# Kernel optimization log

Hardware: AMD Instinct MI355X
Metric: run time of the kernel (lower is better)

Reference implementation:

```python
import jax, jax.numpy as jnp
import numpy as np

NUM_NODES = 4
D = 1024            # hidden dim and dims of s_0, s_1; initial_input_dims = [D, D, 2D]
NUM_OPS = 5         # candidate ops per MixedLayer: linear, relu, tanh, sigmoid, leaky_relu(0.2)
NUM_LAYERS = 18     # sum_{i<4} (i+3)
BATCH = 4096

_ACTS = [
    lambda h: h,
    jax.nn.relu,
    jnp.tanh,
    jax.nn.sigmoid,
    lambda h: jax.nn.leaky_relu(h, 0.2),
]

def setup_inputs() -> dict:
    key = jax.random.key(0)
    ks = jax.random.split(key, 7)
    s_0 = jax.random.normal(ks[0], (BATCH, D), jnp.float32)
    s_1 = jax.random.normal(ks[1], (BATCH, D), jnp.float32)
    genotype = jax.random.uniform(ks[2], (NUM_LAYERS, NUM_OPS), jnp.float32)
    genotype = genotype / genotype.sum(-1, keepdims=True)  # softmax-like arch weights
    scale = 1.0 / np.sqrt(D)
    # 14 layers take a D-dim input; 4 layers (the cat(s_0,s_1) edge of each node) take 2D
    Ws = jax.random.normal(ks[3], (14, NUM_OPS, D, D), jnp.float32) * scale
    Wb = jax.random.normal(ks[4], (4, NUM_OPS, 2 * D, D), jnp.float32) * (scale / np.sqrt(2.0))
    bs = jax.random.normal(ks[5], (NUM_LAYERS, NUM_OPS, D), jnp.float32) * 0.01
    return {"s_0": s_0, "s_1": s_1, "genotype": genotype, "Ws": Ws, "Wb": Wb, "bs": bs}

def _mixed(x, W, b, w):
    # x: [B, in], W: [K, in, D], b: [K, D], w: [K]
    h = jnp.einsum('bi,kio->kbo', x, W) + b[:, None, :]
    out = 0.0
    for k, act in enumerate(_ACTS):
        out = out + w[k] * act(h[k])
    return out

def reference(s_0, s_1, genotype, Ws, Wb, bs):
    states = [s_0, s_1, jnp.concatenate([s_0, s_1], axis=-1)]
    offset, si, bi = 0, 0, 0
    for i in range(NUM_NODES):
        s = 0.0
        for j, cur in enumerate(states):
            l = offset + j
            if j == 2:  # edge from cat(s_0, s_1): input dim 2D
                W = Wb[bi]; bi += 1
            else:
                W = Ws[si]; si += 1
            s = s + _mixed(cur, W, bs[l], genotype[l])
        offset += len(states)
        states.append(s)
    return states[-1]
```

## Files before the change

### kernel.cpp

```cpp
#include <hip/hip_runtime.h>
#include <hip/hip_bf16.h>
#include <cstdint>
#include <cstddef>

typedef __attribute__((ext_vector_type(8))) short bf16x8;
typedef __attribute__((ext_vector_type(4))) float f32x4;

#define DEV __device__ __forceinline__

DEV unsigned short f2bf(float f) {
  unsigned int u = __float_as_uint(f);
  return (unsigned short)((u + 0x7fffu + ((u >> 16) & 1u)) >> 16);
}

DEV void gl_lds16(const unsigned short* g, unsigned short* l) {
  __builtin_amdgcn_global_load_lds(
      (__attribute__((address_space(1))) const void*)g,
      (__attribute__((address_space(3))) void*)l, 16, 0, 0);
}

__global__ __launch_bounds__(256) void cvt_kernel(const float* __restrict__ src,
                                                  unsigned short* __restrict__ dst) {
  size_t i = (size_t)blockIdx.x * 256 + threadIdx.x;
  float4 v = ((const float4*)src)[i];
  ushort4 o;
  o.x = f2bf(v.x); o.y = f2bf(v.y); o.z = f2bf(v.z); o.w = f2bf(v.w);
  ((ushort4*)dst)[i] = o;
}

__global__ __launch_bounds__(256) void zero_kernel(float* __restrict__ p) {
  size_t i = (size_t)blockIdx.x * 256 + threadIdx.x;
  ((float4*)p)[i] = make_float4(0.f, 0.f, 0.f, 0.f);
}

__global__ __launch_bounds__(256) void cvtzero_kernel(float* __restrict__ s,
                                                      unsigned short* __restrict__ dst) {
  size_t i = (size_t)blockIdx.x * 256 + threadIdx.x;
  float4 v = ((float4*)s)[i];
  ushort4 o;
  o.x = f2bf(v.x); o.y = f2bf(v.y); o.z = f2bf(v.z); o.w = f2bf(v.w);
  ((ushort4*)dst)[i] = o;
  ((float4*)s)[i] = make_float4(0.f, 0.f, 0.f, 0.f);
}

__global__ __launch_bounds__(256) void transpose_kernel(const float* __restrict__ src,
                                                        unsigned short* __restrict__ dst,
                                                        int K) {
  __shared__ float tile[64][68];
  const int t = threadIdx.x;
  const int tpm = (K >> 6) * 16;
  const int mat = blockIdx.x / tpm;
  const int r = blockIdx.x % tpm;
  const int tk = r >> 4;
  const int tn = r & 15;
  const size_t sbase = (size_t)mat * K * 1024 + (size_t)tk * 64 * 1024 + (size_t)tn * 64;
#pragma unroll
  for (int p = 0; p < 4; ++p) {
    int row = p * 16 + (t >> 4);
    int c4 = (t & 15) * 4;
    float4 v = *(const float4*)&src[sbase + (size_t)row * 1024 + c4];
    *(float4*)&tile[row][c4] = v;
  }
  __syncthreads();
  const int kbase = tk * 64;
  const size_t dbase = (size_t)mat * 1024 * K + (size_t)(kbase >> 10) * 1024 * 1024 +
                       (size_t)tn * 64 * 1024 + (size_t)(kbase & 1023);
#pragma unroll
  for (int p = 0; p < 4; ++p) {
    int n = p * 16 + (t >> 4);
    int k4 = (t & 15) * 4;
    ushort4 o;
    o.x = f2bf(tile[k4 + 0][n]);
    o.y = f2bf(tile[k4 + 1][n]);
    o.z = f2bf(tile[k4 + 2][n]);
    o.w = f2bf(tile[k4 + 3][n]);
    *(ushort4*)&dst[dbase + (size_t)n * 1024 + k4] = o;
  }
}

struct SegCfg {
  const unsigned short* x;
  const unsigned short* w;
  size_t wops;
  int l;
  int last;
};
struct NodeArgs {
  SegCfg s[7];
  int nseg;
};

#define PIPE_STEP(BUF, SA, SB)                                                   \
  {                                                                              \
    asm volatile("s_waitcnt vmcnt(12)" ::: "memory");                            \
    __builtin_amdgcn_s_barrier();                                                \
    __builtin_amdgcn_sched_barrier(0);                                           \
    bf16x8 af[4], bfr[4];                                                        \
    _Pragma("unroll") for (int mi = 0; mi < 4; ++mi)                             \
        af[mi] = *(const bf16x8*)&lds[(BUF) * 8192 + aof[mi]];                   \
    _Pragma("unroll") for (int ni = 0; ni < 4; ++ni)                             \
        bfr[ni] = *(const bf16x8*)&lds[(BUF) * 8192 + 4096 + bof[ni]];           \
    asm volatile("s_waitcnt lgkmcnt(0)" ::: "memory");                           \
    __builtin_amdgcn_sched_barrier(0);                                           \
    __builtin_amdgcn_s_barrier();                                                \
    __builtin_amdgcn_sched_barrier(0);                                           \
    {                                                                            \
      unsigned short* da = lds + (BUF) * 8192 + t * 8;                           \
      gl_lds16((SA), da);                                                        \
      gl_lds16((SA) + 64 * 1024, da + 2048);                                     \
      gl_lds16((SB), da + 4096);                                                 \
      gl_lds16((SB) + 64 * 1024, da + 6144);                                     \
    }                                                                            \
    _Pragma("unroll") for (int mi = 0; mi < 4; ++mi)                             \
        _Pragma("unroll") for (int ni = 0; ni < 4; ++ni)                         \
            hacc[mi][ni] = __builtin_amdgcn_mfma_f32_16x16x32_bf16(              \
                af[mi], bfr[ni], hacc[mi][ni], 0, 0, 0);                         \
  }

template <int NSEG>
__global__ __launch_bounds__(256, 2) void node_gemm(NodeArgs na,
                                                    const float* __restrict__ genotype,
                                                    const float* __restrict__ bs,
                                                    float* __restrict__ sout) {
  __shared__ unsigned short lds[32768];

  const int t = threadIdx.x;
  const int lane = t & 63;
  const int w = t >> 6;
  const int wm = (w & 1) * 64;
  const int wn = (w >> 1) * 64;
  const int bn = blockIdx.x * 128;
  const int bm = blockIdx.y * 128;
  const int kop = blockIdx.z;
  const int l15 = lane & 15;
  const int l16 = lane >> 4;

  const int srow = ((t >> 5) << 3) | (t & 7);
  const int schunk = (t >> 3) & 3;
  const size_t aoffg = (size_t)(bm + srow) * 1024 + schunk * 8;
  const size_t boffg = (size_t)(bn + srow) * 1024 + schunk * 8;

  int aof[4], bof[4];
#pragma unroll
  for (int mi = 0; mi < 4; ++mi) {
    int r = wm + mi * 16 + l15;
    aof[mi] = (r >> 3) * 256 + l16 * 64 + (r & 7) * 8;
  }
#pragma unroll
  for (int ni = 0; ni < 4; ++ni) {
    int r = wn + ni * 16 + l15;
    bof[ni] = (r >> 3) * 256 + l16 * 64 + (r & 7) * 8;
  }

  float br[NSEG][4];
  float wl[NSEG];
#pragma unroll
  for (int e = 0; e < NSEG; ++e) {
    const int l = na.s[e].l;
    wl[e] = genotype[l * 5 + kop];
#pragma unroll
    for (int ni = 0; ni < 4; ++ni)
      br[e][ni] = bs[((size_t)l * 5 + kop) * 1024 + bn + wn + ni * 16 + l15];
  }

  f32x4 sacc[4][4];
  f32x4 hacc[4][4];
#pragma unroll
  for (int mi = 0; mi < 4; ++mi)
#pragma unroll
    for (int ni = 0; ni < 4; ++ni) {
      sacc[mi][ni] = (f32x4){0.f, 0.f, 0.f, 0.f};
      hacc[mi][ni] = (f32x4){0.f, 0.f, 0.f, 0.f};
    }

  {
    const unsigned short* pa0 = na.s[0].x + aoffg;
    const unsigned short* pb0 = na.s[0].w + (size_t)kop * na.s[0].wops + boffg;
#pragma unroll
    for (int i = 0; i < 4; ++i) {
      unsigned short* da = lds + i * 8192 + t * 8;
      gl_lds16(pa0 + i * 32, da);
      gl_lds16(pa0 + i * 32 + 64 * 1024, da + 2048);
      gl_lds16(pb0 + i * 32, da + 4096);
      gl_lds16(pb0 + i * 32 + 64 * 1024, da + 6144);
    }
  }

#pragma unroll
  for (int e = 0; e < NSEG; ++e) {
    const unsigned short* pa = na.s[e].x + aoffg;
    const unsigned short* pb = na.s[e].w + (size_t)kop * na.s[e].wops + boffg;
    const int en = (e + 1 < NSEG) ? e + 1 : 0;
    const unsigned short* pna = na.s[en].x + aoffg;
    const unsigned short* pnb = na.s[en].w + (size_t)kop * na.s[en].wops + boffg;

#pragma unroll 1
    for (int m = 0; m < 8; ++m) {
      const unsigned short* spa = (m < 7) ? (pa + (size_t)(4 * m + 4) * 32) : pna;
      const unsigned short* spb = (m < 7) ? (pb + (size_t)(4 * m + 4) * 32) : pnb;
      PIPE_STEP(0, spa, spb)
      PIPE_STEP(1, spa + 32, spb + 32)
      PIPE_STEP(2, spa + 64, spb + 64)
      PIPE_STEP(3, spa + 96, spb + 96)
    }

    if (na.s[e].last) {
      const float wlk = wl[e];
#pragma unroll
      for (int ni = 0; ni < 4; ++ni) {
        const float bias = br[e][ni];
#pragma unroll
        for (int mi = 0; mi < 4; ++mi)
#pragma unroll
          for (int i = 0; i < 4; ++i) {
            float h = hacc[mi][ni][i] + bias;
            float a;
            if (kop == 0) a = h;
            else if (kop == 1) a = fmaxf(h, 0.f);
            else if (kop == 2) a = 1.f - 2.f / (__expf(2.f * h) + 1.f);
            else if (kop == 3) a = 1.f / (1.f + __expf(-h));
            else a = (h > 0.f) ? h : 0.2f * h;
            sacc[mi][ni][i] += wlk * a;
            hacc[mi][ni][i] = 0.f;
          }
      }
    }
  }

#pragma unroll
  for (int mi = 0; mi < 4; ++mi)
#pragma unroll
    for (int ni = 0; ni < 4; ++ni)
#pragma unroll
      for (int i = 0; i < 4; ++i) {
        const int row = bm + wm + mi * 16 + l16 * 4 + i;
        const int col = bn + wn + ni * 16 + l15;
        unsafeAtomicAdd(&sout[(size_t)row * 1024 + col], sacc[mi][ni][i]);
      }
}

extern "C" void kernel_launch(void* const* d_in, const int* in_sizes, int n_in,
                              void* d_out, int out_size, void* d_ws, size_t ws_size,
                              hipStream_t stream) {
  const float* s0 = (const float*)d_in[0];
  const float* s1 = (const float*)d_in[1];
  const float* geno = (const float*)d_in[2];
  const float* Ws = (const float*)d_in[3];
  const float* Wb = (const float*)d_in[4];
  const float* bs = (const float*)d_in[5];

  unsigned short* WsT = (unsigned short*)d_ws;
  unsigned short* WbT = WsT + 70ull * 1024 * 1024;
  unsigned short* S0 = WbT + 20ull * 2048 * 1024;
  unsigned short* S1 = S0 + 4096ull * 1024;
  unsigned short* T0 = S1 + 4096ull * 1024;
  unsigned short* T1 = T0 + 4096ull * 1024;
  unsigned short* T2 = T1 + 4096ull * 1024;
  float* S = (float*)(T2 + 4096ull * 1024);

  cvt_kernel<<<4096, 256, 0, stream>>>(s0, S0);
  cvt_kernel<<<4096, 256, 0, stream>>>(s1, S1);
  zero_kernel<<<4096, 256, 0, stream>>>(S);
  zero_kernel<<<4096, 256, 0, stream>>>((float*)d_out);
  transpose_kernel<<<70 * 256, 256, 0, stream>>>(Ws, WsT, 1024);
  transpose_kernel<<<20 * 512, 256, 0, stream>>>(Wb, WbT, 2048);

  auto SS = [&](const unsigned short* x, int si, int l) {
    SegCfg c;
    c.x = x;
    c.w = WsT + (size_t)si * 5 * 1024 * 1024;
    c.wops = (size_t)1024 * 1024;
    c.l = l; c.last = 1;
    return c;
  };
  auto BH = [&](int bi, int half, int l) {
    SegCfg c;
    c.x = half ? S1 : S0;
    c.w = WbT + (size_t)bi * 5 * 2048 * 1024 + (size_t)half * 1024 * 1024;
    c.wops = (size_t)2048 * 1024;
    c.l = l; c.last = half;
    return c;
  };

  dim3 grid(8, 32, 5);
  {
    NodeArgs a{}; a.nseg = 4;
    a.s[0] = SS(S0, 0, 0); a.s[1] = SS(S1, 1, 1);
    a.s[2] = BH(0, 0, 2); a.s[3] = BH(0, 1, 2);
    node_gemm<4><<<grid, 256, 0, stream>>>(a, geno, bs, S);
    cvtzero_kernel<<<4096, 256, 0, stream>>>(S, T0);
  }
  {
    NodeArgs a{}; a.nseg = 5;
    a.s[0] = SS(S0, 2, 3); a.s[1] = SS(S1, 3, 4);
    a.s[2] = BH(1, 0, 5); a.s[3] = BH(1, 1, 5);
    a.s[4] = SS(T0, 4, 6);
    node_gemm<5><<<grid, 256, 0, stream>>>(a, geno, bs, S);
    cvtzero_kernel<<<4096, 256, 0, stream>>>(S, T1);
  }
  {
    NodeArgs a{}; a.nseg = 6;
    a.s[0] = SS(S0, 5, 7); a.s[1] = SS(S1, 6, 8);
    a.s[2] = BH(2, 0, 9); a.s[3] = BH(2, 1, 9);
    a.s[4] = SS(T0, 7, 10); a.s[5] = SS(T1, 8, 11);
    node_gemm<6><<<grid, 256, 0, stream>>>(a, geno, bs, S);
    cvtzero_kernel<<<4096, 256, 0, stream>>>(S, T2);
  }
  {
    NodeArgs a{}; a.nseg = 7;
    a.s[0] = SS(S0, 9, 12); a.s[1] = SS(S1, 10, 13);
    a.s[2] = BH(3, 0, 14); a.s[3] = BH(3, 1, 14);
    a.s[4] = SS(T0, 11, 15); a.s[5] = SS(T1, 12, 16); a.s[6] = SS(T2, 13, 17);
    node_gemm<7><<<grid, 256, 0, stream>>>(a, geno, bs, (float*)d_out);
  }
}
```

Baseline: 2.483 ms.

## Double-buffer MFMA fragments in registers and use one barrier per k-step

Restructures the LDS pipeline so each k-step issues the next global-to-LDS copy, prefetches the next buffer's fragments into a second register set, and runs MFMAs on the current set. This needs one barrier per step instead of two. MFMAs run at raised wave priority via s_setprio. Bias values are staged once in LDS instead of being held in per-segment registers, which lowers register pressure. The epilogue trigger now assumes segment index 2 is the only non-final segment, and the deeper prefetch raises register use.

```diff
diff --git a/kernel.cpp b/kernel.cpp
--- a/kernel.cpp
+++ b/kernel.cpp
@@ -90,31 +90,31 @@
   int nseg;
 };
 
-#define PIPE_STEP(BUF, SA, SB)                                                   \
-  {                                                                              \
-    asm volatile("s_waitcnt vmcnt(12)" ::: "memory");                            \
-    __builtin_amdgcn_s_barrier();                                                \
-    __builtin_amdgcn_sched_barrier(0);                                           \
-    bf16x8 af[4], bfr[4];                                                        \
-    _Pragma("unroll") for (int mi = 0; mi < 4; ++mi)                             \
-        af[mi] = *(const bf16x8*)&lds[(BUF) * 8192 + aof[mi]];                   \
-    _Pragma("unroll") for (int ni = 0; ni < 4; ++ni)                             \
-        bfr[ni] = *(const bf16x8*)&lds[(BUF) * 8192 + 4096 + bof[ni]];           \
-    asm volatile("s_waitcnt lgkmcnt(0)" ::: "memory");                           \
-    __builtin_amdgcn_sched_barrier(0);                                           \
-    __builtin_amdgcn_s_barrier();                                                \
-    __builtin_amdgcn_sched_barrier(0);                                           \
-    {                                                                            \
-      unsigned short* da = lds + (BUF) * 8192 + t * 8;                           \
-      gl_lds16((SA), da);                                                        \
-      gl_lds16((SA) + 64 * 1024, da + 2048);                                     \
-      gl_lds16((SB), da + 4096);                                                 \
-      gl_lds16((SB) + 64 * 1024, da + 6144);                                     \
-    }                                                                            \
-    _Pragma("unroll") for (int mi = 0; mi < 4; ++mi)                             \
-        _Pragma("unroll") for (int ni = 0; ni < 4; ++ni)                         \
-            hacc[mi][ni] = __builtin_amdgcn_mfma_f32_16x16x32_bf16(              \
-                af[mi], bfr[ni], hacc[mi][ni], 0, 0, 0);                         \
+#define ITER(J, CA, CB, NA, NB, SPA, SPB)                                      \
+  {                                                                            \
+    asm volatile("s_waitcnt vmcnt(8)" ::: "memory");                           \
+    __builtin_amdgcn_s_barrier();                                              \
+    {                                                                          \
+      unsigned short* da = lds + (J) * 8192 + t * 8;                           \
+      gl_lds16((SPA), da);                                                     \
+      gl_lds16((SPA) + 64 * 1024, da + 2048);                                  \
+      gl_lds16((SPB), da + 4096);                                              \
+      gl_lds16((SPB) + 64 * 1024, da + 6144);                                  \
+    }                                                                          \
+    {                                                                          \
+      const unsigned short* rb = lds + ((((J) + 1) & 3) * 8192);               \
+      _Pragma("unroll") for (int mi = 0; mi < 4; ++mi)                         \
+          NA[mi] = *(const bf16x8*)&rb[aof[mi]];                               \
+      _Pragma("unroll") for (int ni = 0; ni < 4; ++ni)                         \
+          NB[ni] = *(const bf16x8*)&rb[4096 + bof[ni]];                        \
+    }                                                                          \
+    __builtin_amdgcn_s_setprio(1);                                             \
+    _Pragma("unroll") for (int mi = 0; mi < 4; ++mi)                           \
+        _Pragma("unroll") for (int ni = 0; ni < 4; ++ni)                       \
+            hacc[mi][ni] = __builtin_amdgcn_mfma_f32_16x16x32_bf16(            \
+                CA[mi], CB[ni], hacc[mi][ni], 0, 0, 0);                        \
+    __builtin_amdgcn_s_setprio(0);                                             \
+    asm volatile("s_waitcnt lgkmcnt(0)" ::: "memory");                         \
   }
 
 template <int NSEG>
@@ -122,7 +122,8 @@
                                                     const float* __restrict__ genotype,
                                                     const float* __restrict__ bs,
                                                     float* __restrict__ sout) {
-  __shared__ unsigned short lds[32768];
+  __shared__ unsigned short lds[32768 + 2048];
+  float* biasF = (float*)(lds + 32768);
 
   const int t = threadIdx.x;
   const int lane = t & 63;
@@ -135,6 +136,19 @@
   const int l15 = lane & 15;
   const int l16 = lane >> 4;
 
+  if (t < 128) {
+#pragma unroll
+    for (int e = 0; e < NSEG; ++e) {
+      if (e != 2) {
+        biasF[e * 128 + t] = bs[((size_t)na.s[e].l * 5 + kop) * 1024 + bn + t];
+      }
+    }
+  }
+
+  float wl[NSEG];
+#pragma unroll
+  for (int e = 0; e < NSEG; ++e) wl[e] = genotype[na.s[e].l * 5 + kop];
+
   const int srow = ((t >> 5) << 3) | (t & 7);
   const int schunk = (t >> 3) & 3;
   const size_t aoffg = (size_t)(bm + srow) * 1024 + schunk * 8;
@@ -150,17 +164,6 @@
   for (int ni = 0; ni < 4; ++ni) {
     int r = wn + ni * 16 + l15;
     bof[ni] = (r >> 3) * 256 + l16 * 64 + (r & 7) * 8;
-  }
-
-  float br[NSEG][4];
-  float wl[NSEG];
-#pragma unroll
-  for (int e = 0; e < NSEG; ++e) {
-    const int l = na.s[e].l;
-    wl[e] = genotype[l * 5 + kop];
-#pragma unroll
-    for (int ni = 0; ni < 4; ++ni)
-      br[e][ni] = bs[((size_t)l * 5 + kop) * 1024 + bn + wn + ni * 16 + l15];
   }
 
   f32x4 sacc[4][4];
@@ -186,6 +189,15 @@
     }
   }
 
+  bf16x8 fAa[4], fAb[4], fBa[4], fBb[4];
+  asm volatile("s_waitcnt vmcnt(12)" ::: "memory");
+  __builtin_amdgcn_s_barrier();
+#pragma unroll
+  for (int mi = 0; mi < 4; ++mi) fAa[mi] = *(const bf16x8*)&lds[aof[mi]];
+#pragma unroll
+  for (int ni = 0; ni < 4; ++ni) fAb[ni] = *(const bf16x8*)&lds[4096 + bof[ni]];
+  asm volatile("s_waitcnt lgkmcnt(0)" ::: "memory");
+
 #pragma unroll
   for (int e = 0; e < NSEG; ++e) {
     const unsigned short* pa = na.s[e].x + aoffg;
@@ -198,17 +210,17 @@
     for (int m = 0; m < 8; ++m) {
       const unsigned short* spa = (m < 7) ? (pa + (size_t)(4 * m + 4) * 32) : pna;
       const unsigned short* spb = (m < 7) ? (pb + (size_t)(4 * m + 4) * 32) : pnb;
-      PIPE_STEP(0, spa, spb)
-      PIPE_STEP(1, spa + 32, spb + 32)
-      PIPE_STEP(2, spa + 64, spb + 64)
-      PIPE_STEP(3, spa + 96, spb + 96)
-    }
-
-    if (na.s[e].last) {
+      ITER(0, fAa, fAb, fBa, fBb, spa, spb)
+      ITER(1, fBa, fBb, fAa, fAb, spa + 32, spb + 32)
+      ITER(2, fAa, fAb, fBa, fBb, spa + 64, spb + 64)
+      ITER(3, fBa, fBb, fAa, fAb, spa + 96, spb + 96)
+    }
+
+    if (e != 2) {
       const float wlk = wl[e];
 #pragma unroll
       for (int ni = 0; ni < 4; ++ni) {
-        const float bias = br[e][ni];
+        const float bias = biasF[e * 128 + wn + ni * 16 + l15];
 #pragma unroll
         for (int mi = 0; mi < 4; ++mi)
 #pragma unroll
```

New measurement: 2.860 ms. +15.2%, slower.
